# Performance work log

Measured on AMD Instinct MI355X. Metric: run time of the kernel, lower is better.

The kernel has to match this reference:

```python
import jax, jax.numpy as jnp
import numpy as np

N_HEADS = 16
HEAD_DIM = 64
HIDDEN = N_HEADS * HEAD_DIM


def setup_inputs() -> dict:
    key = jax.random.key(0)
    ks = jax.random.split(key, 10)
    B, F, T = 2, 2048, 2048
    std = 0.02
    inp = {
        "from_tensor": jax.random.normal(ks[0], (B, F, HIDDEN), dtype=jnp.float32),
        "to_tensor": jax.random.normal(ks[1], (B, T, HIDDEN), dtype=jnp.float32),
        "attention_mask": jax.random.randint(ks[2], (B, F, T), 0, 2, dtype=jnp.int32),
        "Wq": jax.random.normal(ks[3], (HIDDEN, HIDDEN), dtype=jnp.float32) * std,
        "bq": jnp.zeros((HIDDEN,), dtype=jnp.float32),
        "Wk": jax.random.normal(ks[4], (HIDDEN, HIDDEN), dtype=jnp.float32) * std,
        "bk": jnp.zeros((HIDDEN,), dtype=jnp.float32),
        "Wv": jax.random.normal(ks[5], (HIDDEN, HIDDEN), dtype=jnp.float32) * std,
        "bv": jnp.zeros((HIDDEN,), dtype=jnp.float32),
    }
    return inp


def reference(from_tensor, to_tensor, attention_mask, Wq, bq, Wk, bk, Wv, bv):
    B, F, _ = from_tensor.shape
    T = to_tensor.shape[1]
    N, H = N_HEADS, HEAD_DIM

    # QKV projections (no activations: query/key/value act fns are None)
    q = (from_tensor @ Wq + bq).reshape(B, F, N, H)
    k = (to_tensor @ Wk + bk).reshape(B, T, N, H)
    v = (to_tensor @ Wv + bv).reshape(B, T, N, H)

    scores = jnp.einsum('BFNH,BTNH->BNFT', q, k) * (1.0 / np.sqrt(float(H)))
    # additive mask: mask [B,F,T] -> [B,1,F,T]; 0 entries get -10000
    adder = (1.0 - attention_mask.astype(jnp.float32))[:, None, :, :] * -10000.0
    scores = scores + adder
    probs = jax.nn.softmax(scores, axis=-1)  # dropout skipped (inference)

    context = jnp.einsum('BNFT,BTNH->BFNH', probs, v)
    return context.reshape(B, F, N * H)
```

## Files before the change

### kernel.cpp

```cpp
#include <hip/hip_runtime.h>


typedef short v8s __attribute__((ext_vector_type(8)));
typedef float v4f __attribute__((ext_vector_type(4)));
typedef unsigned short u16;
typedef unsigned int   u32;
typedef unsigned long long u64;

constexpr float QSCALE = 0.18033688011112042f;

__device__ __forceinline__ u16 f2bf(float f) {
    u32 u = __builtin_bit_cast(u32, f);
    u += 0x7fffu + ((u >> 16) & 1u);
    return (u16)(u >> 16);
}

__device__ __forceinline__ u32 pack_trunc(float a, float b) {
    u32 ua = __builtin_bit_cast(u32, a);
    u32 ub = __builtin_bit_cast(u32, b);
    return (ua >> 16) | (ub & 0xffff0000u);
}

__device__ __forceinline__ v8s ld8(const u16* p) {
    return *reinterpret_cast<const v8s*>(p);
}

__device__ __forceinline__ void async16(const void* g, void* l) {
    __builtin_amdgcn_global_load_lds(
        (const __attribute__((address_space(1))) u32*)g,
        (__attribute__((address_space(3))) u32*)l, 16, 0, 0);
}

__global__ __launch_bounds__(256) void prep(
    const float* __restrict__ from, const float* __restrict__ to,
    u16* __restrict__ Xf, u16* __restrict__ Xt,
    const float* __restrict__ Wq, const float* __restrict__ Wk, const float* __restrict__ Wv,
    u16* __restrict__ Wqt, u16* __restrict__ Wkt, u16* __restrict__ Wvt,
    const int* __restrict__ mask, u64* __restrict__ words) {
    __shared__ float tile[32][33];
    const int bid = blockIdx.x, tid = threadIdx.x;
    if (bid < 8192) {
        int i = bid * 256 + tid;
        const float4* s;
        ushort4* d;
        int j;
        if (i < 1048576) { s = (const float4*)from; d = (ushort4*)Xf; j = i; }
        else             { s = (const float4*)to;   d = (ushort4*)Xt; j = i - 1048576; }
        float4 v = s[j];
        ushort4 o;
        o.x = f2bf(v.x); o.y = f2bf(v.y); o.z = f2bf(v.z); o.w = f2bf(v.w);
        d[j] = o;
    } else if (bid < 11264) {
        const int r = bid - 8192;
        const int zz = r >> 10, rem = r & 1023;
        const float* W = zz == 0 ? Wq : (zz == 1 ? Wk : Wv);
        u16* Wt = zz == 0 ? Wqt : (zz == 1 ? Wkt : Wvt);
        const int tx = tid & 31, ty = tid >> 5;
        const int n0 = (rem & 31) * 32, k0 = (rem >> 5) * 32;
        for (int i = 0; i < 4; i++)
            tile[ty + i * 8][tx] = W[(size_t)(k0 + ty + i * 8) * 1024 + n0 + tx];
        __syncthreads();
        for (int i = 0; i < 4; i++)
            Wt[(size_t)(n0 + ty + i * 8) * 1024 + k0 + tx] = f2bf(tile[tx][ty + i * 8]);
    } else {
        int g = (bid - 11264) * 256 + tid;
        int w = g >> 6, lane = g & 63;
        int v = mask[(size_t)w * 64 + lane];
        u64 bits = __ballot(v != 0);
        if (lane == 0) words[w] = bits;
    }
}

__global__ __launch_bounds__(256) void gemm_qkv(
    const u16* __restrict__ Xf, const u16* __restrict__ Xt,
    const u16* __restrict__ Wqt, const u16* __restrict__ Wkt, const u16* __restrict__ Wvt,
    const float* __restrict__ bq, const float* __restrict__ bk, const float* __restrict__ bv,
    u16* __restrict__ Qb, u16* __restrict__ Kb, u16* __restrict__ Vtb) {
    const int z = blockIdx.z;
    const u16* A      = z == 0 ? Xf : Xt;
    const u16* Bt     = z == 0 ? Wqt : (z == 1 ? Wkt : Wvt);
    const float* bias = z == 0 ? bq : (z == 1 ? bk : bv);
    u16* C            = z == 0 ? Qb : (z == 1 ? Kb : Vtb);
    const int mode    = (z == 2);
    const float sc    = (z == 0) ? QSCALE : 1.0f;

    __shared__ u16 As[128 * 32];
    __shared__ u16 Bs[128 * 32];
    const uint4* Ag = reinterpret_cast<const uint4*>(A);
    const uint4* Bg = reinterpret_cast<const uint4*>(Bt);

    const int tid = threadIdx.x;
    const int lane = tid & 63, wave = tid >> 6;
    const int quad = lane >> 4, l16 = lane & 15;
    const int wm = wave >> 1, wn = wave & 1;
    const int m0 = blockIdx.x * 128, n0 = blockIdx.y * 128;

    const int cg  = (lane & 3) ^ ((lane >> 3) & 3);
    const int sw8 = (quad ^ ((l16 >> 1) & 3)) * 8;

    const int r0 = (wave * 2 + 0) * 16 + (lane >> 2);
    const int r1 = (wave * 2 + 1) * 16 + (lane >> 2);
    const uint4* ap0 = Ag + (size_t)(m0 + r0) * 128 + cg;
    const uint4* ap1 = Ag + (size_t)(m0 + r1) * 128 + cg;
    const uint4* bp0 = Bg + (size_t)(n0 + r0) * 128 + cg;
    const uint4* bp1 = Bg + (size_t)(n0 + r1) * 128 + cg;

    v4f acc[4][4];
    for (int i = 0; i < 4; i++)
        for (int j = 0; j < 4; j++) acc[i][j] = (v4f)0.0f;

    for (int k0 = 0; k0 < 32; k0++) {
        __syncthreads();
        async16(ap0, As + (wave * 2 + 0) * 512); ap0 += 4;
        async16(ap1, As + (wave * 2 + 1) * 512); ap1 += 4;
        async16(bp0, Bs + (wave * 2 + 0) * 512); bp0 += 4;
        async16(bp1, Bs + (wave * 2 + 1) * 512); bp1 += 4;
        __syncthreads();

        v8s af[4], bf[4];
        #pragma unroll
        for (int mt = 0; mt < 4; mt++) af[mt] = ld8(&As[(wm * 64 + mt * 16 + l16) * 32 + sw8]);
        #pragma unroll
        for (int nt = 0; nt < 4; nt++) bf[nt] = ld8(&Bs[(wn * 64 + nt * 16 + l16) * 32 + sw8]);
        #pragma unroll
        for (int mt = 0; mt < 4; mt++)
            #pragma unroll
            for (int nt = 0; nt < 4; nt++)
                acc[mt][nt] = __builtin_amdgcn_mfma_f32_16x16x32_bf16(af[mt], bf[nt], acc[mt][nt], 0, 0, 0);
    }

    #pragma unroll
    for (int nt = 0; nt < 4; nt++) {
        const int col = n0 + wn * 64 + nt * 16 + l16;
        const float bvv = bias[col];
        #pragma unroll
        for (int mt = 0; mt < 4; mt++) {
            const int mbase = m0 + wm * 64 + mt * 16 + quad * 4;
            if (mode == 0) {
                for (int r = 0; r < 4; r++)
                    C[(size_t)(mbase + r) * 1024 + col] = f2bf((acc[mt][nt][r] + bvv) * sc);
            } else {
                const int b = mbase >> 11, t = mbase & 2047;
                const int head = col >> 6, h = col & 63;
                ushort4 pk;
                pk.x = f2bf(acc[mt][nt][0] + bvv);
                pk.y = f2bf(acc[mt][nt][1] + bvv);
                pk.z = f2bf(acc[mt][nt][2] + bvv);
                pk.w = f2bf(acc[mt][nt][3] + bvv);
                *reinterpret_cast<ushort4*>(&C[(size_t)((b * 16 + head) * 64 + h) * 2048 + t]) = pk;
            }
        }
    }
}

__global__ __launch_bounds__(256, 4) void attn_fused(
    const u16* __restrict__ Qb, const u16* __restrict__ Kb,
    const u16* __restrict__ Vtb, const u64* __restrict__ mw,
    float* __restrict__ out, float* __restrict__ O1,
    float* __restrict__ l0w, float* __restrict__ l1w) {
    __shared__ u16 Ks[2][64][32];
    __shared__ u16 Vs[2][64][32];
    __shared__ u32 Ps[4][32 * 36];

    const int tid = threadIdx.x;
    const int lane = tid & 63, wave = tid >> 6;
    const int quad = lane >> 4, l16 = lane & 15;
    const int b = blockIdx.x >> 4, head = blockIdx.x & 15;
    const int f0 = blockIdx.y * 128;
    const int thalf = blockIdx.z;
    const int tbase = thalf * 1024;

    const uint4* Kg = reinterpret_cast<const uint4*>(Kb);
    const uint4* Vg = reinterpret_cast<const uint4*>(Vtb);
    const size_t vbase4 = (size_t)(b * 16 + head) * 64 * 256;

    const int cg  = (lane & 3) ^ ((lane >> 3) & 3);
    const int sw8 = (quad ^ ((l16 >> 1) & 3)) * 8;

    v8s qf[2][2];
    #pragma unroll
    for (int kk = 0; kk < 2; kk++)
        #pragma unroll
        for (int qh = 0; qh < 2; qh++)
            qf[kk][qh] = ld8(Qb + ((size_t)(b * 2048 + f0 + wave * 32 + qh * 16 + l16) * 16 + head) * 64
                                + kk * 32 + quad * 8);

    v8s ones;
    #pragma unroll
    for (int i = 0; i < 8; i++) ones[i] = (short)0x3F80;

    const int kr0 = ((wave * 2 + 0) * 64 + lane) >> 2;
    const int kr1 = ((wave * 2 + 1) * 64 + lane) >> 2;
    const uint4* kp0 = Kg + ((size_t)(b * 2048 + tbase + (kr0 & 63)) * 16 + head) * 8 + (kr0 >> 6) * 4 + cg;
    const uint4* kp1 = Kg + ((size_t)(b * 2048 + tbase + (kr1 & 63)) * 16 + head) * 8 + (kr1 >> 6) * 4 + cg;
    const uint4* vp0 = Vg + vbase4 + (size_t)(kr0 & 63) * 256 + (tbase >> 3) + (kr0 >> 6) * 4 + cg;
    const uint4* vp1 = Vg + vbase4 + (size_t)(kr1 & 63) * 256 + (tbase >> 3) + (kr1 >> 6) * 4 + cg;
    const int dK0 = (wave * 2 + 0) * 512, dK1 = (wave * 2 + 1) * 512;

    v4f accO[2][4], accL[2];
    #pragma unroll
    for (int qh = 0; qh < 2; qh++) {
        accL[qh] = (v4f)0.0f;
        for (int ht = 0; ht < 4; ht++) accO[qh][ht] = (v4f)0.0f;
    }

    u32* myPs = Ps[wave];
    const u64* mrow = mw + (size_t)(b * 2048 + f0 + wave * 32 + l16) * 32 + thalf * 16;

    for (int it = 0; it < 16; it++) {
        __syncthreads();
        async16(kp0, (u16*)Ks + dK0); kp0 += 8192;
        async16(kp1, (u16*)Ks + dK1); kp1 += 8192;
        async16(vp0, (u16*)Vs + dK0); vp0 += 8;
        async16(vp1, (u16*)Vs + dK1); vp1 += 8;
        __syncthreads();

        v4f s[2][4];
        #pragma unroll
        for (int qh = 0; qh < 2; qh++)
            for (int mt = 0; mt < 4; mt++) s[qh][mt] = (v4f)0.0f;
        #pragma unroll
        for (int kk = 0; kk < 2; kk++) {
            v8s kf[4];
            #pragma unroll
            for (int mt = 0; mt < 4; mt++) kf[mt] = ld8(&Ks[kk][mt * 16 + l16][sw8]);
            #pragma unroll
            for (int qh = 0; qh < 2; qh++)
                #pragma unroll
                for (int mt = 0; mt < 4; mt++)
                    s[qh][mt] = __builtin_amdgcn_mfma_f32_16x16x32_bf16(kf[mt], qf[kk][qh], s[qh][mt], 0, 0, 0);
        }

        u32 pk[2][8];
        #pragma unroll
        for (int qh = 0; qh < 2; qh++) {
            const u64 w = mrow[qh * 512 + it];
            const u32 lo = (u32)(w >> (quad * 4));
            const u32 hi = (u32)(w >> (quad * 4 + 32));
            #pragma unroll
            for (int mt = 0; mt < 4; mt++) {
                const u32 bits = ((mt & 2) ? hi : lo) >> ((mt & 1) * 16);
                float p[4];
                #pragma unroll
                for (int r = 0; r < 4; r++) {
                    const float e = __builtin_amdgcn_exp2f(s[qh][mt][r]);
                    p[r] = ((bits >> r) & 1u) ? e : 0.0f;
                }
                pk[qh][mt * 2]     = pack_trunc(p[0], p[1]);
                pk[qh][mt * 2 + 1] = pack_trunc(p[2], p[3]);
            }
        }

        #pragma unroll
        for (int qh = 0; qh < 2; qh++) {
            const int row = qh * 16 + l16;
            #pragma unroll
            for (int mt = 0; mt < 4; mt++)
                *reinterpret_cast<uint2*>(&myPs[row * 36 + mt * 8 + quad * 2]) =
                    make_uint2(pk[qh][mt * 2], pk[qh][mt * 2 + 1]);
        }

        #pragma unroll
        for (int kk = 0; kk < 2; kk++) {
            v8s vf[4];
            #pragma unroll
            for (int ht = 0; ht < 4; ht++) vf[ht] = ld8(&Vs[kk][ht * 16 + l16][sw8]);
            #pragma unroll
            for (int qh = 0; qh < 2; qh++) {
                const v8s pf = *reinterpret_cast<const v8s*>(
                    &myPs[(qh * 16 + l16) * 36 + kk * 16 + quad * 4]);
                #pragma unroll
                for (int ht = 0; ht < 4; ht++)
                    accO[qh][ht] = __builtin_amdgcn_mfma_f32_16x16x32_bf16(vf[ht], pf, accO[qh][ht], 0, 0, 0);
                accL[qh] = __builtin_amdgcn_mfma_f32_16x16x32_bf16(ones, pf, accL[qh], 0, 0, 0);
            }
        }
    }

    float* dst = thalf ? O1 : out;
    float* lws = thalf ? l1w : l0w;
    #pragma unroll
    for (int qh = 0; qh < 2; qh++) {
        const int row = b * 2048 + f0 + wave * 32 + qh * 16 + l16;
        if (quad == 0) lws[(size_t)row * 16 + head] = accL[qh][0];
        const size_t ro = (size_t)row * 1024 + head * 64;
        #pragma unroll
        for (int ht = 0; ht < 4; ht++)
            *reinterpret_cast<float4*>(&dst[ro + ht * 16 + quad * 4]) =
                *reinterpret_cast<float4*>(&accO[qh][ht]);
    }
}

__global__ __launch_bounds__(256) void reduce_out(
    float* __restrict__ out, const float* __restrict__ O1,
    const float* __restrict__ l0w, const float* __restrict__ l1w) {
    const int i4 = blockIdx.x * 256 + threadIdx.x;
    const int flat = i4 * 4;
    const int row = flat >> 10, head = (flat >> 6) & 15;
    float4 a = reinterpret_cast<float4*>(out)[i4];
    const float4 c = reinterpret_cast<const float4*>(O1)[i4];
    const float inv = 1.0f / (l0w[row * 16 + head] + l1w[row * 16 + head]);
    a.x = (a.x + c.x) * inv;
    a.y = (a.y + c.y) * inv;
    a.z = (a.z + c.z) * inv;
    a.w = (a.w + c.w) * inv;
    reinterpret_cast<float4*>(out)[i4] = a;
}

extern "C" void kernel_launch(void* const* d_in, const int* in_sizes, int n_in,
                              void* d_out, int out_size, void* d_ws, size_t ws_size,
                              hipStream_t stream) {
    const float* from = (const float*)d_in[0];
    const float* to   = (const float*)d_in[1];
    const int*   mask = (const int*)d_in[2];
    const float* Wq = (const float*)d_in[3];
    const float* bq = (const float*)d_in[4];
    const float* Wk = (const float*)d_in[5];
    const float* bk = (const float*)d_in[6];
    const float* Wv = (const float*)d_in[7];
    const float* bv = (const float*)d_in[8];
    float* out = (float*)d_out;

    u16* Xf  = (u16*)d_ws;
    u16* Xt  = Xf  + 4194304;
    u16* Wqt = Xt  + 4194304;
    u16* Wkt = Wqt + 1048576;
    u16* Wvt = Wkt + 1048576;
    u16* Qb  = Wvt + 1048576;
    u16* Kb  = Qb  + 4194304;
    u16* Vtb = Kb  + 4194304;
    u64* mwords = (u64*)(Vtb + 4194304);

    float* O1  = (float*)d_ws;
    float* l0w = (float*)Wqt;
    float* l1w = l0w + 65536;

    prep<<<44032, 256, 0, stream>>>(from, to, Xf, Xt, Wq, Wk, Wv, Wqt, Wkt, Wvt, mask, mwords);

    gemm_qkv<<<dim3(32, 8, 3), 256, 0, stream>>>(Xf, Xt, Wqt, Wkt, Wvt, bq, bk, bv, Qb, Kb, Vtb);

    attn_fused<<<dim3(32, 16, 2), 256, 0, stream>>>(Qb, Kb, Vtb, mwords, out, O1, l0w, l1w);

    reduce_out<<<4096, 256, 0, stream>>>(out, O1, l0w, l1w);
}
```

Measured before the change: 238.0 us.

## Merge T-split attention into one 8-wave block with in-LDS combine, deepen GEMM K-step

The attention kernel now runs both key-halves inside one 512-thread block: waves 0-3 stage K tiles and waves 4-7 stage V tiles for both halves. The two partial results are combined through LDS at the end, which removes the separate reduce kernel and the global round trip of partial outputs and row sums. The QKV GEMM loads a 64-wide K slice per barrier pair instead of 32, halving the number of synchronisations. In exchange, the attention grid has half as many blocks, each using more LDS and registers, which may reduce occupancy and load balance.

Result: faster. 226.5 us (-4.8%).

```diff
diff --git a/kernel.cpp b/kernel.cpp
--- a/kernel.cpp
+++ b/kernel.cpp
@@ -84,8 +84,8 @@
     const int mode    = (z == 2);
     const float sc    = (z == 0) ? QSCALE : 1.0f;
 
-    __shared__ u16 As[128 * 32];
-    __shared__ u16 Bs[128 * 32];
+    __shared__ u16 As[2][128][32];
+    __shared__ u16 Bs[2][128][32];
     const uint4* Ag = reinterpret_cast<const uint4*>(A);
     const uint4* Bg = reinterpret_cast<const uint4*>(Bt);
 
@@ -98,35 +98,55 @@
     const int cg  = (lane & 3) ^ ((lane >> 3) & 3);
     const int sw8 = (quad ^ ((l16 >> 1) & 3)) * 8;
 
-    const int r0 = (wave * 2 + 0) * 16 + (lane >> 2);
-    const int r1 = (wave * 2 + 1) * 16 + (lane >> 2);
-    const uint4* ap0 = Ag + (size_t)(m0 + r0) * 128 + cg;
-    const uint4* ap1 = Ag + (size_t)(m0 + r1) * 128 + cg;
-    const uint4* bp0 = Bg + (size_t)(n0 + r0) * 128 + cg;
-    const uint4* bp1 = Bg + (size_t)(n0 + r1) * 128 + cg;
+    const int gi0 = wave * 4;
+    const uint4 *ap0, *ap1, *ap2, *ap3, *bp0, *bp1, *bp2, *bp3;
+    {
+        const int rl = lane >> 2;
+        const int rb0 = ((gi0 + 0) & 7) * 16 + rl, kh0 = (gi0 + 0) >> 3;
+        const int rb1 = ((gi0 + 1) & 7) * 16 + rl, kh1 = (gi0 + 1) >> 3;
+        const int rb2 = ((gi0 + 2) & 7) * 16 + rl, kh2 = (gi0 + 2) >> 3;
+        const int rb3 = ((gi0 + 3) & 7) * 16 + rl, kh3 = (gi0 + 3) >> 3;
+        ap0 = Ag + (size_t)(m0 + rb0) * 128 + kh0 * 4 + cg;
+        ap1 = Ag + (size_t)(m0 + rb1) * 128 + kh1 * 4 + cg;
+        ap2 = Ag + (size_t)(m0 + rb2) * 128 + kh2 * 4 + cg;
+        ap3 = Ag + (size_t)(m0 + rb3) * 128 + kh3 * 4 + cg;
+        bp0 = Bg + (size_t)(n0 + rb0) * 128 + kh0 * 4 + cg;
+        bp1 = Bg + (size_t)(n0 + rb1) * 128 + kh1 * 4 + cg;
+        bp2 = Bg + (size_t)(n0 + rb2) * 128 + kh2 * 4 + cg;
+        bp3 = Bg + (size_t)(n0 + rb3) * 128 + kh3 * 4 + cg;
+    }
+    u16* Asl = (u16*)As + gi0 * 512;
+    u16* Bsl = (u16*)Bs + gi0 * 512;
 
     v4f acc[4][4];
     for (int i = 0; i < 4; i++)
         for (int j = 0; j < 4; j++) acc[i][j] = (v4f)0.0f;
 
-    for (int k0 = 0; k0 < 32; k0++) {
-        __syncthreads();
-        async16(ap0, As + (wave * 2 + 0) * 512); ap0 += 4;
-        async16(ap1, As + (wave * 2 + 1) * 512); ap1 += 4;
-        async16(bp0, Bs + (wave * 2 + 0) * 512); bp0 += 4;
-        async16(bp1, Bs + (wave * 2 + 1) * 512); bp1 += 4;
-        __syncthreads();
-
-        v8s af[4], bf[4];
-        #pragma unroll
-        for (int mt = 0; mt < 4; mt++) af[mt] = ld8(&As[(wm * 64 + mt * 16 + l16) * 32 + sw8]);
-        #pragma unroll
-        for (int nt = 0; nt < 4; nt++) bf[nt] = ld8(&Bs[(wn * 64 + nt * 16 + l16) * 32 + sw8]);
-        #pragma unroll
-        for (int mt = 0; mt < 4; mt++)
-            #pragma unroll
-            for (int nt = 0; nt < 4; nt++)
-                acc[mt][nt] = __builtin_amdgcn_mfma_f32_16x16x32_bf16(af[mt], bf[nt], acc[mt][nt], 0, 0, 0);
+    for (int k0 = 0; k0 < 16; k0++) {
+        __syncthreads();
+        async16(ap0, Asl);        ap0 += 8;
+        async16(ap1, Asl + 512);  ap1 += 8;
+        async16(ap2, Asl + 1024); ap2 += 8;
+        async16(ap3, Asl + 1536); ap3 += 8;
+        async16(bp0, Bsl);        bp0 += 8;
+        async16(bp1, Bsl + 512);  bp1 += 8;
+        async16(bp2, Bsl + 1024); bp2 += 8;
+        async16(bp3, Bsl + 1536); bp3 += 8;
+        __syncthreads();
+
+        #pragma unroll
+        for (int kk = 0; kk < 2; kk++) {
+            v8s af[4], bf[4];
+            #pragma unroll
+            for (int mt = 0; mt < 4; mt++) af[mt] = ld8(&As[kk][wm * 64 + mt * 16 + l16][sw8]);
+            #pragma unroll
+            for (int nt = 0; nt < 4; nt++) bf[nt] = ld8(&Bs[kk][wn * 64 + nt * 16 + l16][sw8]);
+            #pragma unroll
+            for (int mt = 0; mt < 4; mt++)
+                #pragma unroll
+                for (int nt = 0; nt < 4; nt++)
+                    acc[mt][nt] = __builtin_amdgcn_mfma_f32_16x16x32_bf16(af[mt], bf[nt], acc[mt][nt], 0, 0, 0);
+        }
     }
 
     #pragma unroll
@@ -153,22 +173,20 @@
     }
 }
 
-__global__ __launch_bounds__(256, 4) void attn_fused(
+__global__ __launch_bounds__(512, 4) void attn_fused(
     const u16* __restrict__ Qb, const u16* __restrict__ Kb,
     const u16* __restrict__ Vtb, const u64* __restrict__ mw,
-    float* __restrict__ out, float* __restrict__ O1,
-    float* __restrict__ l0w, float* __restrict__ l1w) {
-    __shared__ u16 Ks[2][64][32];
-    __shared__ u16 Vs[2][64][32];
-    __shared__ u32 Ps[4][32 * 36];
+    float* __restrict__ out) {
+    __shared__ u16 Ks[2][2][64][32];
+    __shared__ u16 Vs[2][2][64][32];
+    __shared__ u32 Ps[8 * 1152];
 
     const int tid = threadIdx.x;
     const int lane = tid & 63, wave = tid >> 6;
     const int quad = lane >> 4, l16 = lane & 15;
+    const int fwave = wave & 3, tw = wave >> 2;
     const int b = blockIdx.x >> 4, head = blockIdx.x & 15;
     const int f0 = blockIdx.y * 128;
-    const int thalf = blockIdx.z;
-    const int tbase = thalf * 1024;
 
     const uint4* Kg = reinterpret_cast<const uint4*>(Kb);
     const uint4* Vg = reinterpret_cast<const uint4*>(Vtb);
@@ -182,20 +200,36 @@
     for (int kk = 0; kk < 2; kk++)
         #pragma unroll
         for (int qh = 0; qh < 2; qh++)
-            qf[kk][qh] = ld8(Qb + ((size_t)(b * 2048 + f0 + wave * 32 + qh * 16 + l16) * 16 + head) * 64
+            qf[kk][qh] = ld8(Qb + ((size_t)(b * 2048 + f0 + fwave * 32 + qh * 16 + l16) * 16 + head) * 64
                                 + kk * 32 + quad * 8);
 
     v8s ones;
     #pragma unroll
     for (int i = 0; i < 8; i++) ones[i] = (short)0x3F80;
 
-    const int kr0 = ((wave * 2 + 0) * 64 + lane) >> 2;
-    const int kr1 = ((wave * 2 + 1) * 64 + lane) >> 2;
-    const uint4* kp0 = Kg + ((size_t)(b * 2048 + tbase + (kr0 & 63)) * 16 + head) * 8 + (kr0 >> 6) * 4 + cg;
-    const uint4* kp1 = Kg + ((size_t)(b * 2048 + tbase + (kr1 & 63)) * 16 + head) * 8 + (kr1 >> 6) * 4 + cg;
-    const uint4* vp0 = Vg + vbase4 + (size_t)(kr0 & 63) * 256 + (tbase >> 3) + (kr0 >> 6) * 4 + cg;
-    const uint4* vp1 = Vg + vbase4 + (size_t)(kr1 & 63) * 256 + (tbase >> 3) + (kr1 >> 6) * 4 + cg;
-    const int dK0 = (wave * 2 + 0) * 512, dK1 = (wave * 2 + 1) * 512;
+    const uint4 *sp0, *sp1, *sp2, *sp3;
+    u16 *sd;
+    size_t sinc;
+    {
+        const int rl = lane >> 2;
+        if (wave < 4) {
+            const int g0 = wave * 4;
+            sd = (u16*)Ks + g0 * 512;
+            sinc = 8192;
+            #define KPTR(g) (Kg + ((size_t)(b * 2048 + ((g) >> 3) * 1024 + ((g) & 3) * 16 + rl) * 16 + head) * 8 \
+                                + (((g) >> 2) & 1) * 4 + cg)
+            sp0 = KPTR(g0); sp1 = KPTR(g0 + 1); sp2 = KPTR(g0 + 2); sp3 = KPTR(g0 + 3);
+            #undef KPTR
+        } else {
+            const int g0 = (wave - 4) * 4;
+            sd = (u16*)Vs + g0 * 512;
+            sinc = 8;
+            #define VPTR(g) (Vg + vbase4 + (size_t)(((g) & 3) * 16 + rl) * 256 + ((g) >> 3) * 128 \
+                                + (((g) >> 2) & 1) * 4 + cg)
+            sp0 = VPTR(g0); sp1 = VPTR(g0 + 1); sp2 = VPTR(g0 + 2); sp3 = VPTR(g0 + 3);
+            #undef VPTR
+        }
+    }
 
     v4f accO[2][4], accL[2];
     #pragma unroll
@@ -204,15 +238,15 @@
         for (int ht = 0; ht < 4; ht++) accO[qh][ht] = (v4f)0.0f;
     }
 
-    u32* myPs = Ps[wave];
-    const u64* mrow = mw + (size_t)(b * 2048 + f0 + wave * 32 + l16) * 32 + thalf * 16;
+    u32* myPs = Ps + wave * 1152;
+    const u64* mrow = mw + (size_t)(b * 2048 + f0 + fwave * 32 + l16) * 32 + tw * 16;
 
     for (int it = 0; it < 16; it++) {
         __syncthreads();
-        async16(kp0, (u16*)Ks + dK0); kp0 += 8192;
-        async16(kp1, (u16*)Ks + dK1); kp1 += 8192;
-        async16(vp0, (u16*)Vs + dK0); vp0 += 8;
-        async16(vp1, (u16*)Vs + dK1); vp1 += 8;
+        async16(sp0, sd);        sp0 += sinc;
+        async16(sp1, sd + 512);  sp1 += sinc;
+        async16(sp2, sd + 1024); sp2 += sinc;
+        async16(sp3, sd + 1536); sp3 += sinc;
         __syncthreads();
 
         v4f s[2][4];
@@ -223,7 +257,7 @@
         for (int kk = 0; kk < 2; kk++) {
             v8s kf[4];
             #pragma unroll
-            for (int mt = 0; mt < 4; mt++) kf[mt] = ld8(&Ks[kk][mt * 16 + l16][sw8]);
+            for (int mt = 0; mt < 4; mt++) kf[mt] = ld8(&Ks[tw][kk][mt * 16 + l16][sw8]);
             #pragma unroll
             for (int qh = 0; qh < 2; qh++)
                 #pragma unroll
@@ -264,7 +298,7 @@
         for (int kk = 0; kk < 2; kk++) {
             v8s vf[4];
             #pragma unroll
-            for (int ht = 0; ht < 4; ht++) vf[ht] = ld8(&Vs[kk][ht * 16 + l16][sw8]);
+            for (int ht = 0; ht < 4; ht++) vf[ht] = ld8(&Vs[tw][kk][ht * 16 + l16][sw8]);
             #pragma unroll
             for (int qh = 0; qh < 2; qh++) {
                 const v8s pf = *reinterpret_cast<const v8s*>(
@@ -277,34 +311,40 @@
         }
     }
 
-    float* dst = thalf ? O1 : out;
-    float* lws = thalf ? l1w : l0w;
-    #pragma unroll
-    for (int qh = 0; qh < 2; qh++) {
-        const int row = b * 2048 + f0 + wave * 32 + qh * 16 + l16;
-        if (quad == 0) lws[(size_t)row * 16 + head] = accL[qh][0];
-        const size_t ro = (size_t)row * 1024 + head * 64;
-        #pragma unroll
-        for (int ht = 0; ht < 4; ht++)
-            *reinterpret_cast<float4*>(&dst[ro + ht * 16 + quad * 4]) =
-                *reinterpret_cast<float4*>(&accO[qh][ht]);
-    }
-}
-
-__global__ __launch_bounds__(256) void reduce_out(
-    float* __restrict__ out, const float* __restrict__ O1,
-    const float* __restrict__ l0w, const float* __restrict__ l1w) {
-    const int i4 = blockIdx.x * 256 + threadIdx.x;
-    const int flat = i4 * 4;
-    const int row = flat >> 10, head = (flat >> 6) & 15;
-    float4 a = reinterpret_cast<float4*>(out)[i4];
-    const float4 c = reinterpret_cast<const float4*>(O1)[i4];
-    const float inv = 1.0f / (l0w[row * 16 + head] + l1w[row * 16 + head]);
-    a.x = (a.x + c.x) * inv;
-    a.y = (a.y + c.y) * inv;
-    a.z = (a.z + c.z) * inv;
-    a.w = (a.w + c.w) * inv;
-    reinterpret_cast<float4*>(out)[i4] = a;
+    __syncthreads();
+    float* fb = (float*)Ps;
+    if (tw == 1) {
+        float* wdst = fb + fwave * 2304 + lane * 36;
+        #pragma unroll
+        for (int qh = 0; qh < 2; qh++)
+            #pragma unroll
+            for (int ht = 0; ht < 4; ht++)
+                *reinterpret_cast<v4f*>(wdst + (qh * 4 + ht) * 4) = accO[qh][ht];
+        wdst[32] = accL[0][0];
+        wdst[33] = accL[1][0];
+    }
+    __syncthreads();
+    if (tw == 0) {
+        const float* rsrc = fb + fwave * 2304 + lane * 36;
+        float inv[2];
+        #pragma unroll
+        for (int qh = 0; qh < 2; qh++)
+            inv[qh] = 1.0f / (accL[qh][0] + rsrc[32 + qh]);
+        #pragma unroll
+        for (int qh = 0; qh < 2; qh++) {
+            const size_t ro = (size_t)(b * 2048 + f0 + fwave * 32 + qh * 16 + l16) * 1024 + head * 64;
+            #pragma unroll
+            for (int ht = 0; ht < 4; ht++) {
+                const v4f p = *reinterpret_cast<const v4f*>(rsrc + (qh * 4 + ht) * 4);
+                float4 o;
+                o.x = (accO[qh][ht][0] + p[0]) * inv[qh];
+                o.y = (accO[qh][ht][1] + p[1]) * inv[qh];
+                o.z = (accO[qh][ht][2] + p[2]) * inv[qh];
+                o.w = (accO[qh][ht][3] + p[3]) * inv[qh];
+                *reinterpret_cast<float4*>(&out[ro + ht * 16 + quad * 4]) = o;
+            }
+        }
+    }
 }
 
 extern "C" void kernel_launch(void* const* d_in, const int* in_sizes, int n_in,
@@ -331,15 +371,9 @@
     u16* Vtb = Kb  + 4194304;
     u64* mwords = (u64*)(Vtb + 4194304);
 
-    float* O1  = (float*)d_ws;
-    float* l0w = (float*)Wqt;
-    float* l1w = l0w + 65536;
-
     prep<<<44032, 256, 0, stream>>>(from, to, Xf, Xt, Wq, Wk, Wv, Wqt, Wkt, Wvt, mask, mwords);
 
     gemm_qkv<<<dim3(32, 8, 3), 256, 0, stream>>>(Xf, Xt, Wqt, Wkt, Wvt, bq, bk, bv, Qb, Kb, Vtb);
 
-    attn_fused<<<dim3(32, 16, 2), 256, 0, stream>>>(Qb, Kb, Vtb, mwords, out, O1, l0w, l1w);
-
-    reduce_out<<<4096, 256, 0, stream>>>(out, O1, l0w, l1w);
-}
+    attn_fused<<<dim3(32, 16), 512, 0, stream>>>(Qb, Kb, Vtb, mwords, out);
+}
```
